# Performance work log

Measured on AMD Instinct MI355X. Metric: run time of the kernel, lower is better.

The kernel has to match this reference:

```python
import jax, jax.numpy as jnp
import numpy as np

N = 12288
IN_DIM = 256
HID = 64
E = 393216


def _gcn_edges(edge_index, n):
    # add self-loops, compute symmetric normalization (PyG GCNConv default)
    src = jnp.concatenate([edge_index[0], jnp.arange(n, dtype=edge_index.dtype)])
    dst = jnp.concatenate([edge_index[1], jnp.arange(n, dtype=edge_index.dtype)])
    deg = jax.ops.segment_sum(jnp.ones_like(src, dtype=jnp.float32), dst, num_segments=n)
    dinv = jnp.where(deg > 0, jax.lax.rsqrt(deg), 0.0)
    norm = dinv[src] * dinv[dst]  # [E+N]
    return src, dst, norm


def _conv(h, src, dst, norm, W, b, n):
    # GCNConv: linear transform then normalized sparse aggregation
    h = h @ W
    agg = jax.ops.segment_sum(h[src] * norm[:, None], dst, num_segments=n)
    return agg + b


def setup_inputs() -> dict:
    key = jax.random.key(0)
    ks = jax.random.split(key, 16)
    x = jax.random.normal(ks[0], (N, IN_DIM), dtype=jnp.float32)
    edge_index = jax.random.randint(ks[1], (2, E), 0, N, dtype=jnp.int32)
    s = 0.05
    p = {
        'enc_W1': jax.random.normal(ks[2], (IN_DIM, HID), jnp.float32) * s,
        'enc_b1': jnp.zeros((HID,), jnp.float32),
        'enc_W2': jax.random.normal(ks[3], (HID, HID), jnp.float32) * s,
        'enc_b2': jnp.zeros((HID,), jnp.float32),
        'd1_W1': jax.random.normal(ks[4], (HID // 2, HID), jnp.float32) * s,
        'd1_b1': jnp.zeros((HID,), jnp.float32),
        'd1_W2': jax.random.normal(ks[5], (HID, IN_DIM), jnp.float32) * s,
        'd1_b2': jnp.zeros((IN_DIM,), jnp.float32),
        'd2_W1': jax.random.normal(ks[6], (HID // 2, HID), jnp.float32) * s,
        'd2_b1': jnp.zeros((HID,), jnp.float32),
        'd2_W2': jax.random.normal(ks[7], (HID, IN_DIM), jnp.float32) * s,
        'd2_b2': jnp.zeros((IN_DIM,), jnp.float32),
        's_W': jax.random.normal(ks[8], (HID // 2, HID), jnp.float32) * s,
        's_b': jnp.zeros((HID,), jnp.float32),
    }
    return dict(x=x, edge_index=edge_index, **p)


def reference(x, edge_index, enc_W1, enc_b1, enc_W2, enc_b2,
              d1_W1, d1_b1, d1_W2, d1_b2, d2_W1, d2_b1, d2_W2, d2_b2,
              s_W, s_b):
    n = x.shape[0]
    src, dst, norm = _gcn_edges(edge_index, n)

    def encoder(h):
        h = jax.nn.relu(_conv(h, src, dst, norm, enc_W1, enc_b1, n))
        return _conv(h, src, dst, norm, enc_W2, enc_b2, n)

    def dec1(h):
        h = jax.nn.relu(_conv(h, src, dst, norm, d1_W1, d1_b1, n))
        return _conv(h, src, dst, norm, d1_W2, d1_b2, n)

    def dec2(h):
        h = jax.nn.relu(_conv(h, src, dst, norm, d2_W1, d2_b1, n))
        return _conv(h, src, dst, norm, d2_W2, d2_b2, n)

    z = encoder(x)
    # counterfactual: flip sensitive attribute (column 0)
    x_cf = x.at[:, 0].set(1.0 - x[:, 0])
    z_cf = encoder(x_cf)

    h = z.shape[1] // 2
    z_s, z_ns = z[:, :h], z[:, h:]
    z_s_cf = z_cf[:, :h]

    x_s_hat = dec1(z_s)
    x_ns_hat = dec2(z_ns)
    x_s_cf_hat = dec1(z_s_cf)

    # DotProductDecoder: 1-layer GCN then dense inner-product decode (sigmoid_s=False)
    hs = _conv(z_ns, src, dst, norm, s_W, s_b, n)
    s_ = hs @ hs.T  # [N, N]

    return (z_s, z_ns, x_s_hat, x_ns_hat, x_s_cf_hat, s_)
```

## Files before the change

kernel.cpp:

```cpp
#include <hip/hip_runtime.h>

#define N_NODES 12288
#define IN_DIM_ 256
#define HID_ 64
#define E_EDGES 393216
#define TOT_EDGES (E_EDGES + N_NODES)

typedef __attribute__((ext_vector_type(8))) short bf16x8;
typedef __attribute__((ext_vector_type(16))) float f32x16;

__device__ inline unsigned short f2bf_rne(float f) {
  unsigned int u = __float_as_uint(f);
  unsigned int r = u + 0x7fffu + ((u >> 16) & 1u);
  return (unsigned short)(r >> 16);
}
__device__ inline float bf2f(unsigned short h) {
  return __uint_as_float(((unsigned int)h) << 16);
}


__global__ __launch_bounds__(256) void k_init(const float* __restrict__ x,
                                              int* __restrict__ deg,
                                              float* __restrict__ coef) {
  int i = blockIdx.x * 256 + threadIdx.x;
  if (i < N_NODES) {
    deg[i] = 1;
    coef[i] = 1.0f - 2.0f * x[(size_t)i * IN_DIM_];
  }
}

__global__ __launch_bounds__(256) void k_count(const int* __restrict__ dst,
                                               int* __restrict__ deg) {
  int e = blockIdx.x * 256 + threadIdx.x;
  if (e < E_EDGES) atomicAdd(&deg[dst[e]], 1);
}

__global__ __launch_bounds__(1024) void k_scan(const int* __restrict__ deg,
                                               int* __restrict__ rowptr,
                                               int* __restrict__ cursor,
                                               float* __restrict__ dinv) {
  __shared__ int sh[1024];
  const int t = threadIdx.x;
  int loc[12];
  int s = 0;
#pragma unroll
  for (int i = 0; i < 12; i++) {
    int d = deg[t * 12 + i];
    dinv[t * 12 + i] = 1.0f / sqrtf((float)d);
    loc[i] = s;
    s += d;
  }
  sh[t] = s;
  __syncthreads();
  for (int off = 1; off < 1024; off <<= 1) {
    int v = (t >= off) ? sh[t - off] : 0;
    __syncthreads();
    sh[t] += v;
    __syncthreads();
  }
  int base = sh[t] - s;
#pragma unroll
  for (int i = 0; i < 12; i++) {
    int v = base + loc[i];
    rowptr[t * 12 + i] = v;
    cursor[t * 12 + i] = v;
  }
  if (t == 1023) rowptr[N_NODES] = sh[1023];
}

__global__ __launch_bounds__(256) void k_fill(const int* __restrict__ src,
                                              const int* __restrict__ dst,
                                              const float* __restrict__ dinv,
                                              int* __restrict__ cursor,
                                              int* __restrict__ col,
                                              float* __restrict__ wgt) {
  int e = blockIdx.x * 256 + threadIdx.x;
  if (e < E_EDGES) {
    int s = src[e], d = dst[e];
    int pos = atomicAdd(&cursor[d], 1);
    col[pos] = s;
    wgt[pos] = dinv[s] * dinv[d];
  } else if (e < TOT_EDGES) {
    int i = e - E_EDGES;
    int pos = atomicAdd(&cursor[i], 1);
    col[pos] = i;
    float di = dinv[i];
    wgt[pos] = di * di;
  }
}


template <bool BIAS, bool RELU, bool RANK1, bool SPLIT>
__global__ __launch_bounds__(256) void k_agg64(const float* __restrict__ in,
                                               const int* __restrict__ rowptr,
                                               const int* __restrict__ col,
                                               const float* __restrict__ wgt,
                                               const float* __restrict__ bias,
                                               const float* __restrict__ coef,
                                               const float* __restrict__ wrow,
                                               float* __restrict__ out,
                                               float* __restrict__ out2) {
  const int lane = threadIdx.x & 63;
  int node = blockIdx.x * 4 + (threadIdx.x >> 6);
  node = __builtin_amdgcn_readfirstlane(node);
  const int start = rowptr[node];
  const int end = rowptr[node + 1];
  const float wr = RANK1 ? wrow[lane] : 0.0f;
  float a0 = 0.0f, a1 = 0.0f, a2 = 0.0f, a3 = 0.0f;
  int e = start;
  for (; e + 4 <= end; e += 4) {
    int c0 = col[e + 0], c1 = col[e + 1], c2 = col[e + 2], c3 = col[e + 3];
    float w0 = wgt[e + 0], w1 = wgt[e + 1], w2 = wgt[e + 2], w3 = wgt[e + 3];
    float v0 = in[(size_t)c0 * 64 + lane];
    float v1 = in[(size_t)c1 * 64 + lane];
    float v2 = in[(size_t)c2 * 64 + lane];
    float v3 = in[(size_t)c3 * 64 + lane];
    if (RANK1) {
      v0 = fmaf(coef[c0], wr, v0);
      v1 = fmaf(coef[c1], wr, v1);
      v2 = fmaf(coef[c2], wr, v2);
      v3 = fmaf(coef[c3], wr, v3);
    }
    a0 = fmaf(w0, v0, a0);
    a1 = fmaf(w1, v1, a1);
    a2 = fmaf(w2, v2, a2);
    a3 = fmaf(w3, v3, a3);
  }
  for (; e < end; ++e) {
    int c = col[e];
    float v = in[(size_t)c * 64 + lane];
    if (RANK1) v = fmaf(coef[c], wr, v);
    a0 = fmaf(wgt[e], v, a0);
  }
  float acc = (a0 + a1) + (a2 + a3);
  if (BIAS) acc += bias[lane];
  if (RELU) acc = fmaxf(acc, 0.0f);
  if (SPLIT) {
    if (lane < 32)
      out[(size_t)node * 32 + lane] = acc;
    else
      out2[(size_t)node * 32 + (lane - 32)] = acc;
  } else {
    out[(size_t)node * 64 + lane] = acc;
  }
}

template <bool BIAS>
__global__ __launch_bounds__(256) void k_agg32(const float* __restrict__ in,
                                               const int* __restrict__ rowptr,
                                               const int* __restrict__ col,
                                               const float* __restrict__ wgt,
                                               const float* __restrict__ bias,
                                               float* __restrict__ out) {
  const int lane = threadIdx.x & 31;
  const int node = blockIdx.x * 8 + (threadIdx.x >> 5);
  const int start = rowptr[node];
  const int end = rowptr[node + 1];
  float a0 = 0.0f, a1 = 0.0f, a2 = 0.0f, a3 = 0.0f;
  int e = start;
  for (; e + 4 <= end; e += 4) {
    int c0 = col[e + 0], c1 = col[e + 1], c2 = col[e + 2], c3 = col[e + 3];
    float w0 = wgt[e + 0], w1 = wgt[e + 1], w2 = wgt[e + 2], w3 = wgt[e + 3];
    a0 = fmaf(w0, in[(size_t)c0 * 32 + lane], a0);
    a1 = fmaf(w1, in[(size_t)c1 * 32 + lane], a1);
    a2 = fmaf(w2, in[(size_t)c2 * 32 + lane], a2);
    a3 = fmaf(w3, in[(size_t)c3 * 32 + lane], a3);
  }
  for (; e < end; ++e) a0 = fmaf(wgt[e], in[(size_t)col[e] * 32 + lane], a0);
  float acc = (a0 + a1) + (a2 + a3);
  if (BIAS) acc += bias[lane];
  out[(size_t)node * 32 + lane] = acc;
}


template <int K, int NF, int LDW, int RPT, bool BIAS, bool RELU>
__global__ __launch_bounds__(256) void k_gemm(const float* __restrict__ A,
                                              const float* __restrict__ W,
                                              const float* __restrict__ bias,
                                              float* __restrict__ C) {
  __shared__ float Ws[K * NF];
  for (int i = threadIdx.x; i < K * NF; i += 256) {
    int k = i / NF, c2 = i % NF;
    Ws[i] = W[k * LDW + c2];
  }
  __syncthreads();
  constexpr int G = 256 / NF;
  const int c = threadIdx.x % NF;
  const int rg = threadIdx.x / NF;
  const int r0 = blockIdx.x * (G * RPT) + rg * RPT;
  float acc[RPT];
#pragma unroll
  for (int i = 0; i < RPT; i++) acc[i] = 0.0f;
#pragma unroll 4
  for (int k = 0; k < K; ++k) {
    float wv = Ws[k * NF + c];
#pragma unroll
    for (int i = 0; i < RPT; i++)
      acc[i] = fmaf(A[(size_t)(r0 + i) * K + k], wv, acc[i]);
  }
  float b = BIAS ? bias[c] : 0.0f;
#pragma unroll
  for (int i = 0; i < RPT; i++) {
    float v = acc[i] + b;
    if (RELU) v = fmaxf(v, 0.0f);
    C[(size_t)(r0 + i) * NF + c] = v;
  }
}

__global__ __launch_bounds__(256) void k_gemm_hs(const float* __restrict__ A,
                                                 const float* __restrict__ W,
                                                 const float* __restrict__ bias,
                                                 unsigned short* __restrict__ hi,
                                                 unsigned short* __restrict__ lo) {
  __shared__ float Ws[32 * 64];
  for (int i = threadIdx.x; i < 32 * 64; i += 256) {
    int k = i / 64, c2 = i % 64;
    Ws[i] = W[k * 64 + c2];
  }
  __syncthreads();
  const int c = threadIdx.x % 64;
  const int rg = threadIdx.x / 64;
  const int r0 = blockIdx.x * 32 + rg * 8;
  float acc[8];
#pragma unroll
  for (int i = 0; i < 8; i++) acc[i] = 0.0f;
#pragma unroll 4
  for (int k = 0; k < 32; ++k) {
    float wv = Ws[k * 64 + c];
#pragma unroll
    for (int i = 0; i < 8; i++)
      acc[i] = fmaf(A[(size_t)(r0 + i) * 32 + k], wv, acc[i]);
  }
  float b = bias[c];
#pragma unroll
  for (int i = 0; i < 8; i++) {
    float v = acc[i] + b;
    unsigned short h = f2bf_rne(v);
    float l = v - bf2f(h);
    hi[(size_t)(r0 + i) * 64 + c] = h;
    lo[(size_t)(r0 + i) * 64 + c] = f2bf_rne(l);
  }
}


__global__ __launch_bounds__(256) void k_syrk_mfma(
    const unsigned short* __restrict__ hhi, const unsigned short* __restrict__ hlo,
    float* __restrict__ out) {
  const int tid = threadIdx.x;
  const int lane = tid & 63;
  const int wave = tid >> 6;
  const int wy = wave >> 1, wx = wave & 1;
  const int m = lane & 31;
  const int koff = (lane >> 5) * 8;
  const size_t rb = (size_t)blockIdx.y * 128 + wy * 64;
  const size_t cb = (size_t)blockIdx.x * 128 + wx * 64;
  f32x16 acc[2][2];
#pragma unroll
  for (int i = 0; i < 2; i++)
#pragma unroll
    for (int j = 0; j < 2; j++) acc[i][j] = (f32x16)(0.0f);
#pragma unroll
  for (int k0 = 0; k0 < 64; k0 += 16) {
    bf16x8 ah[2], al[2], bh[2], bl[2];
#pragma unroll
    for (int t = 0; t < 2; t++) {
      size_t ra = (rb + t * 32 + m) * 64 + k0 + koff;
      ah[t] = *(const bf16x8*)(hhi + ra);
      al[t] = *(const bf16x8*)(hlo + ra);
      size_t rc = (cb + t * 32 + m) * 64 + k0 + koff;
      bh[t] = *(const bf16x8*)(hhi + rc);
      bl[t] = *(const bf16x8*)(hlo + rc);
    }
#pragma unroll
    for (int i = 0; i < 2; i++)
#pragma unroll
      for (int j = 0; j < 2; j++) {
        acc[i][j] = __builtin_amdgcn_mfma_f32_32x32x16_bf16(ah[i], bh[j], acc[i][j], 0, 0, 0);
        acc[i][j] = __builtin_amdgcn_mfma_f32_32x32x16_bf16(ah[i], bl[j], acc[i][j], 0, 0, 0);
        acc[i][j] = __builtin_amdgcn_mfma_f32_32x32x16_bf16(al[i], bh[j], acc[i][j], 0, 0, 0);
      }
  }
  const int rowoff = 4 * (lane >> 5);
  const int colc = lane & 31;
#pragma unroll
  for (int i = 0; i < 2; i++)
#pragma unroll
    for (int j = 0; j < 2; j++)
#pragma unroll
      for (int r = 0; r < 16; r++) {
        size_t row = rb + i * 32 + (r & 3) + 8 * (r >> 2) + rowoff;
        out[row * 12288 + cb + j * 32 + colc] = acc[i][j][r];
      }
}


extern "C" void kernel_launch(void* const* d_in, const int* in_sizes, int n_in,
                              void* d_out, int out_size, void* d_ws,
                              size_t ws_size, hipStream_t stream) {
  (void)in_sizes; (void)n_in; (void)out_size; (void)ws_size;
  const float* x = (const float*)d_in[0];
  const int* ei = (const int*)d_in[1];
  const int* src = ei;
  const int* dst = ei + E_EDGES;
  const float* eW1 = (const float*)d_in[2];
  const float* eb1 = (const float*)d_in[3];
  const float* eW2 = (const float*)d_in[4];
  const float* eb2 = (const float*)d_in[5];
  const float* d1W1 = (const float*)d_in[6];
  const float* d1b1 = (const float*)d_in[7];
  const float* d1W2 = (const float*)d_in[8];
  const float* d1b2 = (const float*)d_in[9];
  const float* d2W1 = (const float*)d_in[10];
  const float* d2b1 = (const float*)d_in[11];
  const float* d2W2 = (const float*)d_in[12];
  const float* d2b2 = (const float*)d_in[13];
  const float* sW = (const float*)d_in[14];
  const float* sb = (const float*)d_in[15];

  float* out = (float*)d_out;
  float* out_zs = out;
  float* out_zns = out + 393216;
  float* out_xs = out + 786432;
  float* out_xns = out + 3932160;
  float* out_xscf = out + 7077888;
  float* out_s = out + 10223616;

  char* w = (char*)d_ws;
  size_t o = 0;
  auto alloc = [&](size_t bytes) -> void* {
    void* p = (void*)(w + o);
    o += (bytes + 255) & ~(size_t)255;
    return p;
  };
  int* deg = (int*)alloc(N_NODES * 4);
  int* rowptr = (int*)alloc((N_NODES + 1) * 4);
  int* cursor = (int*)alloc(N_NODES * 4);
  int* col = (int*)alloc(TOT_EDGES * 4);
  float* wgt = (float*)alloc(TOT_EDGES * 4);
  float* dinv = (float*)alloc(N_NODES * 4);
  float* coef = (float*)alloc(N_NODES * 4);
  const size_t B64 = (size_t)N_NODES * 64 * 4;
  const size_t B32 = (size_t)N_NODES * 32 * 4;
  float* slotA = (float*)alloc(B64);
  float* slotB = (float*)alloc(B64);
  float* slotC = (float*)alloc(B64);
  float* slotD = (float*)alloc(B32);
  float* slotE = (float*)alloc(B32);
  unsigned short* hhi = (unsigned short*)alloc((size_t)N_NODES * 64 * 2);
  unsigned short* hlo = (unsigned short*)alloc((size_t)N_NODES * 64 * 2);

  k_init<<<48, 256, 0, stream>>>(x, deg, coef);
  k_count<<<1536, 256, 0, stream>>>(dst, deg);
  k_scan<<<1, 1024, 0, stream>>>(deg, rowptr, cursor, dinv);
  k_fill<<<1584, 256, 0, stream>>>(src, dst, dinv, cursor, col, wgt);

  k_gemm<256, 64, 64, 8, false, false><<<384, 256, 0, stream>>>(x, eW1, nullptr, slotA);
  k_agg64<true, true, false, false><<<3072, 256, 0, stream>>>(slotA, rowptr, col, wgt, eb1, nullptr, nullptr, slotB, nullptr);
  k_agg64<true, true, true, false><<<3072, 256, 0, stream>>>(slotA, rowptr, col, wgt, eb1, coef, eW1, slotC, nullptr);
  k_gemm<64, 64, 64, 8, false, false><<<384, 256, 0, stream>>>(slotB, eW2, nullptr, slotA);
  k_agg64<true, false, false, true><<<3072, 256, 0, stream>>>(slotA, rowptr, col, wgt, eb2, nullptr, nullptr, out_zs, out_zns);
  k_gemm<64, 32, 64, 4, false, false><<<384, 256, 0, stream>>>(slotC, eW2, nullptr, slotD);
  k_agg32<true><<<1536, 256, 0, stream>>>(slotD, rowptr, col, wgt, eb2, slotE);

  k_agg32<false><<<1536, 256, 0, stream>>>(out_zs, rowptr, col, wgt, nullptr, slotD);
  k_gemm<32, 64, 64, 8, true, true><<<384, 256, 0, stream>>>(slotD, d1W1, d1b1, slotB);
  k_agg64<false, false, false, false><<<3072, 256, 0, stream>>>(slotB, rowptr, col, wgt, nullptr, nullptr, nullptr, slotC, nullptr);
  k_gemm<64, 256, 256, 8, true, false><<<1536, 256, 0, stream>>>(slotC, d1W2, d1b2, out_xs);

  k_agg32<false><<<1536, 256, 0, stream>>>(slotE, rowptr, col, wgt, nullptr, slotD);
  k_gemm<32, 64, 64, 8, true, true><<<384, 256, 0, stream>>>(slotD, d1W1, d1b1, slotB);
  k_agg64<false, false, false, false><<<3072, 256, 0, stream>>>(slotB, rowptr, col, wgt, nullptr, nullptr, nullptr, slotC, nullptr);
  k_gemm<64, 256, 256, 8, true, false><<<1536, 256, 0, stream>>>(slotC, d1W2, d1b2, out_xscf);

  k_agg32<false><<<1536, 256, 0, stream>>>(out_zns, rowptr, col, wgt, nullptr, slotE);

  k_gemm_hs<<<384, 256, 0, stream>>>(slotE, sW, sb, hhi, hlo);

  k_gemm<32, 64, 64, 8, true, true><<<384, 256, 0, stream>>>(slotE, d2W1, d2b1, slotB);
  k_agg64<false, false, false, false><<<3072, 256, 0, stream>>>(slotB, rowptr, col, wgt, nullptr, nullptr, nullptr, slotC, nullptr);
  k_gemm<64, 256, 256, 8, true, false><<<1536, 256, 0, stream>>>(slotC, d2W2, d2b2, out_xns);

  k_syrk_mfma<<<dim3(96, 96), 256, 0, stream>>>(hhi, hlo, out_s);
}
```

Measured before the change: 1.076 ms.

## Batch parallel encoder/decoder branches into multi-slice kernels and unroll gathers by 8

The independent branches (factual and counterfactual encoder, the three decoder paths) are merged into single launches that use blockIdx.y as a slice selector. This cuts the kernel count from about 22 to 12 and gives each launch more parallel blocks. The edge-gather loops in the aggregation kernels are unrolled from 4 to 8 to keep more independent loads in flight. The cost is more intermediate buffers and some per-slice pointer selection in each kernel.

```diff
diff --git a/kernel.cpp b/kernel.cpp
--- a/kernel.cpp
+++ b/kernel.cpp
@@ -90,14 +90,12 @@
 }
 
 
-template <bool BIAS, bool RELU, bool RANK1, bool SPLIT>
+template <bool BIAS, bool RELU, bool SPLIT>
 __global__ __launch_bounds__(256) void k_agg64(const float* __restrict__ in,
                                                const int* __restrict__ rowptr,
                                                const int* __restrict__ col,
                                                const float* __restrict__ wgt,
                                                const float* __restrict__ bias,
-                                               const float* __restrict__ coef,
-                                               const float* __restrict__ wrow,
                                                float* __restrict__ out,
                                                float* __restrict__ out2) {
   const int lane = threadIdx.x & 63;
@@ -105,32 +103,33 @@
   node = __builtin_amdgcn_readfirstlane(node);
   const int start = rowptr[node];
   const int end = rowptr[node + 1];
-  const float wr = RANK1 ? wrow[lane] : 0.0f;
   float a0 = 0.0f, a1 = 0.0f, a2 = 0.0f, a3 = 0.0f;
   int e = start;
-  for (; e + 4 <= end; e += 4) {
+  for (; e + 8 <= end; e += 8) {
     int c0 = col[e + 0], c1 = col[e + 1], c2 = col[e + 2], c3 = col[e + 3];
+    int c4 = col[e + 4], c5 = col[e + 5], c6 = col[e + 6], c7 = col[e + 7];
     float w0 = wgt[e + 0], w1 = wgt[e + 1], w2 = wgt[e + 2], w3 = wgt[e + 3];
+    float w4 = wgt[e + 4], w5 = wgt[e + 5], w6 = wgt[e + 6], w7 = wgt[e + 7];
     float v0 = in[(size_t)c0 * 64 + lane];
     float v1 = in[(size_t)c1 * 64 + lane];
     float v2 = in[(size_t)c2 * 64 + lane];
     float v3 = in[(size_t)c3 * 64 + lane];
-    if (RANK1) {
-      v0 = fmaf(coef[c0], wr, v0);
-      v1 = fmaf(coef[c1], wr, v1);
-      v2 = fmaf(coef[c2], wr, v2);
-      v3 = fmaf(coef[c3], wr, v3);
-    }
+    float v4 = in[(size_t)c4 * 64 + lane];
+    float v5 = in[(size_t)c5 * 64 + lane];
+    float v6 = in[(size_t)c6 * 64 + lane];
+    float v7 = in[(size_t)c7 * 64 + lane];
     a0 = fmaf(w0, v0, a0);
     a1 = fmaf(w1, v1, a1);
     a2 = fmaf(w2, v2, a2);
     a3 = fmaf(w3, v3, a3);
+    a0 = fmaf(w4, v4, a0);
+    a1 = fmaf(w5, v5, a1);
+    a2 = fmaf(w6, v6, a2);
+    a3 = fmaf(w7, v7, a3);
   }
   for (; e < end; ++e) {
     int c = col[e];
-    float v = in[(size_t)c * 64 + lane];
-    if (RANK1) v = fmaf(coef[c], wr, v);
-    a0 = fmaf(wgt[e], v, a0);
+    a0 = fmaf(wgt[e], in[(size_t)c * 64 + lane], a0);
   }
   float acc = (a0 + a1) + (a2 + a3);
   if (BIAS) acc += bias[lane];
@@ -143,6 +142,108 @@
   } else {
     out[(size_t)node * 64 + lane] = acc;
   }
+}
+
+__global__ __launch_bounds__(256) void k_agg64_enc(
+    const float* __restrict__ in, const int* __restrict__ rowptr,
+    const int* __restrict__ col, const float* __restrict__ wgt,
+    const float* __restrict__ bias, const float* __restrict__ coef,
+    const float* __restrict__ wrow, float* __restrict__ out0,
+    float* __restrict__ out1) {
+  const int lane = threadIdx.x & 63;
+  int node = blockIdx.x * 4 + (threadIdx.x >> 6);
+  node = __builtin_amdgcn_readfirstlane(node);
+  const int slice = blockIdx.y;
+  const float wr = slice ? wrow[lane] : 0.0f;
+  const int start = rowptr[node];
+  const int end = rowptr[node + 1];
+  float a0 = 0.0f, a1 = 0.0f, a2 = 0.0f, a3 = 0.0f;
+  int e = start;
+  for (; e + 8 <= end; e += 8) {
+    int c0 = col[e + 0], c1 = col[e + 1], c2 = col[e + 2], c3 = col[e + 3];
+    int c4 = col[e + 4], c5 = col[e + 5], c6 = col[e + 6], c7 = col[e + 7];
+    float w0 = wgt[e + 0], w1 = wgt[e + 1], w2 = wgt[e + 2], w3 = wgt[e + 3];
+    float w4 = wgt[e + 4], w5 = wgt[e + 5], w6 = wgt[e + 6], w7 = wgt[e + 7];
+    float v0 = in[(size_t)c0 * 64 + lane];
+    float v1 = in[(size_t)c1 * 64 + lane];
+    float v2 = in[(size_t)c2 * 64 + lane];
+    float v3 = in[(size_t)c3 * 64 + lane];
+    float v4 = in[(size_t)c4 * 64 + lane];
+    float v5 = in[(size_t)c5 * 64 + lane];
+    float v6 = in[(size_t)c6 * 64 + lane];
+    float v7 = in[(size_t)c7 * 64 + lane];
+    v0 = fmaf(coef[c0], wr, v0);
+    v1 = fmaf(coef[c1], wr, v1);
+    v2 = fmaf(coef[c2], wr, v2);
+    v3 = fmaf(coef[c3], wr, v3);
+    v4 = fmaf(coef[c4], wr, v4);
+    v5 = fmaf(coef[c5], wr, v5);
+    v6 = fmaf(coef[c6], wr, v6);
+    v7 = fmaf(coef[c7], wr, v7);
+    a0 = fmaf(w0, v0, a0);
+    a1 = fmaf(w1, v1, a1);
+    a2 = fmaf(w2, v2, a2);
+    a3 = fmaf(w3, v3, a3);
+    a0 = fmaf(w4, v4, a0);
+    a1 = fmaf(w5, v5, a1);
+    a2 = fmaf(w6, v6, a2);
+    a3 = fmaf(w7, v7, a3);
+  }
+  for (; e < end; ++e) {
+    int c = col[e];
+    float v = in[(size_t)c * 64 + lane];
+    v = fmaf(coef[c], wr, v);
+    a0 = fmaf(wgt[e], v, a0);
+  }
+  float acc = (a0 + a1) + (a2 + a3) + bias[lane];
+  acc = fmaxf(acc, 0.0f);
+  (slice ? out1 : out0)[(size_t)node * 64 + lane] = acc;
+}
+
+__global__ __launch_bounds__(256) void k_agg64_dec3(
+    const float* __restrict__ in0, const float* __restrict__ in1,
+    const float* __restrict__ in2, const int* __restrict__ rowptr,
+    const int* __restrict__ col, const float* __restrict__ wgt,
+    float* __restrict__ out0, float* __restrict__ out1,
+    float* __restrict__ out2) {
+  const int lane = threadIdx.x & 63;
+  int node = blockIdx.x * 4 + (threadIdx.x >> 6);
+  node = __builtin_amdgcn_readfirstlane(node);
+  const int slice = blockIdx.y;
+  const float* __restrict__ in = slice == 0 ? in0 : (slice == 1 ? in1 : in2);
+  float* __restrict__ out = slice == 0 ? out0 : (slice == 1 ? out1 : out2);
+  const int start = rowptr[node];
+  const int end = rowptr[node + 1];
+  float a0 = 0.0f, a1 = 0.0f, a2 = 0.0f, a3 = 0.0f;
+  int e = start;
+  for (; e + 8 <= end; e += 8) {
+    int c0 = col[e + 0], c1 = col[e + 1], c2 = col[e + 2], c3 = col[e + 3];
+    int c4 = col[e + 4], c5 = col[e + 5], c6 = col[e + 6], c7 = col[e + 7];
+    float w0 = wgt[e + 0], w1 = wgt[e + 1], w2 = wgt[e + 2], w3 = wgt[e + 3];
+    float w4 = wgt[e + 4], w5 = wgt[e + 5], w6 = wgt[e + 6], w7 = wgt[e + 7];
+    float v0 = in[(size_t)c0 * 64 + lane];
+    float v1 = in[(size_t)c1 * 64 + lane];
+    float v2 = in[(size_t)c2 * 64 + lane];
+    float v3 = in[(size_t)c3 * 64 + lane];
+    float v4 = in[(size_t)c4 * 64 + lane];
+    float v5 = in[(size_t)c5 * 64 + lane];
+    float v6 = in[(size_t)c6 * 64 + lane];
+    float v7 = in[(size_t)c7 * 64 + lane];
+    a0 = fmaf(w0, v0, a0);
+    a1 = fmaf(w1, v1, a1);
+    a2 = fmaf(w2, v2, a2);
+    a3 = fmaf(w3, v3, a3);
+    a0 = fmaf(w4, v4, a0);
+    a1 = fmaf(w5, v5, a1);
+    a2 = fmaf(w6, v6, a2);
+    a3 = fmaf(w7, v7, a3);
+  }
+  for (; e < end; ++e) {
+    int c = col[e];
+    a0 = fmaf(wgt[e], in[(size_t)c * 64 + lane], a0);
+  }
+  float acc = (a0 + a1) + (a2 + a3);
+  out[(size_t)node * 64 + lane] = acc;
 }
 
 template <bool BIAS>
@@ -158,18 +259,57 @@
   const int end = rowptr[node + 1];
   float a0 = 0.0f, a1 = 0.0f, a2 = 0.0f, a3 = 0.0f;
   int e = start;
-  for (; e + 4 <= end; e += 4) {
+  for (; e + 8 <= end; e += 8) {
     int c0 = col[e + 0], c1 = col[e + 1], c2 = col[e + 2], c3 = col[e + 3];
+    int c4 = col[e + 4], c5 = col[e + 5], c6 = col[e + 6], c7 = col[e + 7];
     float w0 = wgt[e + 0], w1 = wgt[e + 1], w2 = wgt[e + 2], w3 = wgt[e + 3];
+    float w4 = wgt[e + 4], w5 = wgt[e + 5], w6 = wgt[e + 6], w7 = wgt[e + 7];
     a0 = fmaf(w0, in[(size_t)c0 * 32 + lane], a0);
     a1 = fmaf(w1, in[(size_t)c1 * 32 + lane], a1);
     a2 = fmaf(w2, in[(size_t)c2 * 32 + lane], a2);
     a3 = fmaf(w3, in[(size_t)c3 * 32 + lane], a3);
+    a0 = fmaf(w4, in[(size_t)c4 * 32 + lane], a0);
+    a1 = fmaf(w5, in[(size_t)c5 * 32 + lane], a1);
+    a2 = fmaf(w6, in[(size_t)c6 * 32 + lane], a2);
+    a3 = fmaf(w7, in[(size_t)c7 * 32 + lane], a3);
   }
   for (; e < end; ++e) a0 = fmaf(wgt[e], in[(size_t)col[e] * 32 + lane], a0);
   float acc = (a0 + a1) + (a2 + a3);
   if (BIAS) acc += bias[lane];
   out[(size_t)node * 32 + lane] = acc;
+}
+
+__global__ __launch_bounds__(256) void k_agg32_b3(
+    const float* __restrict__ in0, const float* __restrict__ in1,
+    const float* __restrict__ in2, const int* __restrict__ rowptr,
+    const int* __restrict__ col, const float* __restrict__ wgt,
+    float* __restrict__ out0, float* __restrict__ out1,
+    float* __restrict__ out2) {
+  const int lane = threadIdx.x & 31;
+  const int node = blockIdx.x * 8 + (threadIdx.x >> 5);
+  const int slice = blockIdx.y;
+  const float* __restrict__ in = slice == 0 ? in0 : (slice == 1 ? in1 : in2);
+  float* __restrict__ out = slice == 0 ? out0 : (slice == 1 ? out1 : out2);
+  const int start = rowptr[node];
+  const int end = rowptr[node + 1];
+  float a0 = 0.0f, a1 = 0.0f, a2 = 0.0f, a3 = 0.0f;
+  int e = start;
+  for (; e + 8 <= end; e += 8) {
+    int c0 = col[e + 0], c1 = col[e + 1], c2 = col[e + 2], c3 = col[e + 3];
+    int c4 = col[e + 4], c5 = col[e + 5], c6 = col[e + 6], c7 = col[e + 7];
+    float w0 = wgt[e + 0], w1 = wgt[e + 1], w2 = wgt[e + 2], w3 = wgt[e + 3];
+    float w4 = wgt[e + 4], w5 = wgt[e + 5], w6 = wgt[e + 6], w7 = wgt[e + 7];
+    a0 = fmaf(w0, in[(size_t)c0 * 32 + lane], a0);
+    a1 = fmaf(w1, in[(size_t)c1 * 32 + lane], a1);
+    a2 = fmaf(w2, in[(size_t)c2 * 32 + lane], a2);
+    a3 = fmaf(w3, in[(size_t)c3 * 32 + lane], a3);
+    a0 = fmaf(w4, in[(size_t)c4 * 32 + lane], a0);
+    a1 = fmaf(w5, in[(size_t)c5 * 32 + lane], a1);
+    a2 = fmaf(w6, in[(size_t)c6 * 32 + lane], a2);
+    a3 = fmaf(w7, in[(size_t)c7 * 32 + lane], a3);
+  }
+  for (; e < end; ++e) a0 = fmaf(wgt[e], in[(size_t)col[e] * 32 + lane], a0);
+  out[(size_t)node * 32 + lane] = (a0 + a1) + (a2 + a3);
 }
 
 
@@ -205,6 +345,105 @@
     if (RELU) v = fmaxf(v, 0.0f);
     C[(size_t)(r0 + i) * NF + c] = v;
   }
+}
+
+__global__ __launch_bounds__(256) void k_gemm_enc2(
+    const float* __restrict__ A0, const float* __restrict__ A1,
+    const float* __restrict__ W, float* __restrict__ C0,
+    float* __restrict__ C1) {
+  __shared__ float Ws[64 * 64];
+  const int slice = blockIdx.y;
+  const float* __restrict__ A = slice ? A1 : A0;
+  for (int i = threadIdx.x; i < 64 * 64; i += 256) Ws[i] = W[i];
+  __syncthreads();
+  const int c = threadIdx.x & 63;
+  const int rg = threadIdx.x >> 6;
+  const int r0 = blockIdx.x * 32 + rg * 8;
+  float acc[8];
+#pragma unroll
+  for (int i = 0; i < 8; i++) acc[i] = 0.0f;
+#pragma unroll 4
+  for (int k = 0; k < 64; ++k) {
+    float wv = Ws[k * 64 + c];
+#pragma unroll
+    for (int i = 0; i < 8; i++)
+      acc[i] = fmaf(A[(size_t)(r0 + i) * 64 + k], wv, acc[i]);
+  }
+  if (slice == 0) {
+#pragma unroll
+    for (int i = 0; i < 8; i++) C0[(size_t)(r0 + i) * 64 + c] = acc[i];
+  } else if (c < 32) {
+#pragma unroll
+    for (int i = 0; i < 8; i++) C1[(size_t)(r0 + i) * 32 + c] = acc[i];
+  }
+}
+
+__global__ __launch_bounds__(256) void k_gemm_u3(
+    const float* __restrict__ A0, const float* __restrict__ A1,
+    const float* __restrict__ A2, const float* __restrict__ W0,
+    const float* __restrict__ W1, const float* __restrict__ W2,
+    const float* __restrict__ b0, const float* __restrict__ b1,
+    const float* __restrict__ b2, float* __restrict__ C0,
+    float* __restrict__ C1, float* __restrict__ C2) {
+  __shared__ float Ws[32 * 64];
+  const int slice = blockIdx.y;
+  const float* __restrict__ A = slice == 0 ? A0 : (slice == 1 ? A1 : A2);
+  const float* __restrict__ W = slice == 0 ? W0 : (slice == 1 ? W1 : W2);
+  const float* __restrict__ bias = slice == 0 ? b0 : (slice == 1 ? b1 : b2);
+  float* __restrict__ C = slice == 0 ? C0 : (slice == 1 ? C1 : C2);
+  for (int i = threadIdx.x; i < 32 * 64; i += 256) Ws[i] = W[i];
+  __syncthreads();
+  const int c = threadIdx.x & 63;
+  const int rg = threadIdx.x >> 6;
+  const int r0 = blockIdx.x * 32 + rg * 8;
+  float acc[8];
+#pragma unroll
+  for (int i = 0; i < 8; i++) acc[i] = 0.0f;
+#pragma unroll 4
+  for (int k = 0; k < 32; ++k) {
+    float wv = Ws[k * 64 + c];
+#pragma unroll
+    for (int i = 0; i < 8; i++)
+      acc[i] = fmaf(A[(size_t)(r0 + i) * 32 + k], wv, acc[i]);
+  }
+  float b = bias[c];
+#pragma unroll
+  for (int i = 0; i < 8; i++) {
+    float v = acc[i] + b;
+    C[(size_t)(r0 + i) * 64 + c] = fmaxf(v, 0.0f);
+  }
+}
+
+__global__ __launch_bounds__(256) void k_gemm_o3(
+    const float* __restrict__ A0, const float* __restrict__ A1,
+    const float* __restrict__ A2, const float* __restrict__ W0,
+    const float* __restrict__ W1, const float* __restrict__ W2,
+    const float* __restrict__ b0, const float* __restrict__ b1,
+    const float* __restrict__ b2, float* __restrict__ C0,
+    float* __restrict__ C1, float* __restrict__ C2) {
+  __shared__ float Ws[64 * 256];
+  const int slice = blockIdx.y;
+  const float* __restrict__ A = slice == 0 ? A0 : (slice == 1 ? A1 : A2);
+  const float* __restrict__ W = slice == 0 ? W0 : (slice == 1 ? W1 : W2);
+  const float* __restrict__ bias = slice == 0 ? b0 : (slice == 1 ? b1 : b2);
+  float* __restrict__ C = slice == 0 ? C0 : (slice == 1 ? C1 : C2);
+  for (int i = threadIdx.x; i < 64 * 256; i += 256) Ws[i] = W[i];
+  __syncthreads();
+  const int c = threadIdx.x;
+  const int r0 = blockIdx.x * 8;
+  float acc[8];
+#pragma unroll
+  for (int i = 0; i < 8; i++) acc[i] = 0.0f;
+#pragma unroll 4
+  for (int k = 0; k < 64; ++k) {
+    float wv = Ws[k * 256 + c];
+#pragma unroll
+    for (int i = 0; i < 8; i++)
+      acc[i] = fmaf(A[(size_t)(r0 + i) * 64 + k], wv, acc[i]);
+  }
+  float b = bias[c];
+#pragma unroll
+  for (int i = 0; i < 8; i++) C[(size_t)(r0 + i) * 256 + c] = acc[i] + b;
 }
 
 __global__ __launch_bounds__(256) void k_gemm_hs(const float* __restrict__ A,
@@ -344,8 +583,14 @@
   float* slotA = (float*)alloc(B64);
   float* slotB = (float*)alloc(B64);
   float* slotC = (float*)alloc(B64);
-  float* slotD = (float*)alloc(B32);
-  float* slotE = (float*)alloc(B32);
+  float* slotU3 = (float*)alloc(B64);
+  float* slotG2 = (float*)alloc(B64);
+  float* slotG3 = (float*)alloc(B64);
+  float* t32 = (float*)alloc(B32);
+  float* zscf = (float*)alloc(B32);
+  float* gs = (float*)alloc(B32);
+  float* gscf = (float*)alloc(B32);
+  float* gns = (float*)alloc(B32);
   unsigned short* hhi = (unsigned short*)alloc((size_t)N_NODES * 64 * 2);
   unsigned short* hlo = (unsigned short*)alloc((size_t)N_NODES * 64 * 2);
 
@@ -355,30 +600,25 @@
   k_fill<<<1584, 256, 0, stream>>>(src, dst, dinv, cursor, col, wgt);
 
   k_gemm<256, 64, 64, 8, false, false><<<384, 256, 0, stream>>>(x, eW1, nullptr, slotA);
-  k_agg64<true, true, false, false><<<3072, 256, 0, stream>>>(slotA, rowptr, col, wgt, eb1, nullptr, nullptr, slotB, nullptr);
-  k_agg64<true, true, true, false><<<3072, 256, 0, stream>>>(slotA, rowptr, col, wgt, eb1, coef, eW1, slotC, nullptr);
-  k_gemm<64, 64, 64, 8, false, false><<<384, 256, 0, stream>>>(slotB, eW2, nullptr, slotA);
-  k_agg64<true, false, false, true><<<3072, 256, 0, stream>>>(slotA, rowptr, col, wgt, eb2, nullptr, nullptr, out_zs, out_zns);
-  k_gemm<64, 32, 64, 4, false, false><<<384, 256, 0, stream>>>(slotC, eW2, nullptr, slotD);
-  k_agg32<true><<<1536, 256, 0, stream>>>(slotD, rowptr, col, wgt, eb2, slotE);
-
-  k_agg32<false><<<1536, 256, 0, stream>>>(out_zs, rowptr, col, wgt, nullptr, slotD);
-  k_gemm<32, 64, 64, 8, true, true><<<384, 256, 0, stream>>>(slotD, d1W1, d1b1, slotB);
-  k_agg64<false, false, false, false><<<3072, 256, 0, stream>>>(slotB, rowptr, col, wgt, nullptr, nullptr, nullptr, slotC, nullptr);
-  k_gemm<64, 256, 256, 8, true, false><<<1536, 256, 0, stream>>>(slotC, d1W2, d1b2, out_xs);
-
-  k_agg32<false><<<1536, 256, 0, stream>>>(slotE, rowptr, col, wgt, nullptr, slotD);
-  k_gemm<32, 64, 64, 8, true, true><<<384, 256, 0, stream>>>(slotD, d1W1, d1b1, slotB);
-  k_agg64<false, false, false, false><<<3072, 256, 0, stream>>>(slotB, rowptr, col, wgt, nullptr, nullptr, nullptr, slotC, nullptr);
-  k_gemm<64, 256, 256, 8, true, false><<<1536, 256, 0, stream>>>(slotC, d1W2, d1b2, out_xscf);
-
-  k_agg32<false><<<1536, 256, 0, stream>>>(out_zns, rowptr, col, wgt, nullptr, slotE);
-
-  k_gemm_hs<<<384, 256, 0, stream>>>(slotE, sW, sb, hhi, hlo);
-
-  k_gemm<32, 64, 64, 8, true, true><<<384, 256, 0, stream>>>(slotE, d2W1, d2b1, slotB);
-  k_agg64<false, false, false, false><<<3072, 256, 0, stream>>>(slotB, rowptr, col, wgt, nullptr, nullptr, nullptr, slotC, nullptr);
-  k_gemm<64, 256, 256, 8, true, false><<<1536, 256, 0, stream>>>(slotC, d2W2, d2b2, out_xns);
+  k_agg64_enc<<<dim3(3072, 2), 256, 0, stream>>>(slotA, rowptr, col, wgt, eb1,
+                                                 coef, eW1, slotB, slotC);
+  k_gemm_enc2<<<dim3(384, 2), 256, 0, stream>>>(slotB, slotC, eW2, slotA, t32);
+  k_agg64<true, false, true><<<3072, 256, 0, stream>>>(slotA, rowptr, col, wgt,
+                                                       eb2, out_zs, out_zns);
+  k_agg32<true><<<1536, 256, 0, stream>>>(t32, rowptr, col, wgt, eb2, zscf);
+
+  k_agg32_b3<<<dim3(1536, 3), 256, 0, stream>>>(out_zs, zscf, out_zns, rowptr,
+                                                col, wgt, gs, gscf, gns);
+  k_gemm_hs<<<384, 256, 0, stream>>>(gns, sW, sb, hhi, hlo);
+  k_gemm_u3<<<dim3(384, 3), 256, 0, stream>>>(gs, gscf, gns, d1W1, d1W1, d2W1,
+                                              d1b1, d1b1, d2b1, slotB, slotC,
+                                              slotU3);
+  k_agg64_dec3<<<dim3(3072, 3), 256, 0, stream>>>(slotB, slotC, slotU3, rowptr,
+                                                  col, wgt, slotA, slotG2,
+                                                  slotG3);
+  k_gemm_o3<<<dim3(1536, 3), 256, 0, stream>>>(slotA, slotG2, slotG3, d1W2,
+                                               d1W2, d2W2, d1b2, d1b2, d2b2,
+                                               out_xs, out_xscf, out_xns);
 
   k_syrk_mfma<<<dim3(96, 96), 256, 0, stream>>>(hhi, hlo, out_s);
 }
```

Result: faster. 999.0 us (-7.1%).
